# Kernel tuning notes

Hardware: AMD Instinct MI355X
Metric: run time of the kernel (lower is better)

## Reference

```python
import jax, jax.numpy as jnp
import numpy as np

N_NODES = 50000
N_EDGES = 200000
IN_DIM = 512
HID = 2000
LAT = 128


def setup_inputs() -> dict:
    key = jax.random.key(0)
    ks = jax.random.split(key, 6)
    x = jax.random.normal(ks[0], (N_NODES, IN_DIM), dtype=jnp.float32)
    edge_index = jax.random.randint(ks[1], (2, N_EDGES), 0, N_NODES, dtype=jnp.int64)
    # glorot-ish scales so ReLU/Sigmoid stay in a sane range
    W1 = jax.random.normal(ks[2], (IN_DIM, HID), dtype=jnp.float32) * (1.0 / np.sqrt(IN_DIM))
    b1 = jnp.zeros((HID,), dtype=jnp.float32)
    W2 = jax.random.normal(ks[3], (HID, LAT), dtype=jnp.float32) * (1.0 / np.sqrt(HID))
    b2 = jnp.zeros((LAT,), dtype=jnp.float32)
    return {"x": x, "edge_index": edge_index, "W1": W1, "b1": b1, "W2": W2, "b2": b2}


def gcn_conv(x, edge_index, W, b):
    """PyG GCNConv: D^-1/2 (A+I) D^-1/2 (X W) + b, unit edge weights."""
    n = x.shape[0]
    loops = jnp.arange(n, dtype=edge_index.dtype)
    row = jnp.concatenate([edge_index[0], loops])  # source nodes
    col = jnp.concatenate([edge_index[1], loops])  # target nodes
    deg = jax.ops.segment_sum(jnp.ones_like(col, dtype=x.dtype), col, num_segments=n)
    dis = jnp.where(deg > 0, jax.lax.rsqrt(deg), 0.0)  # deg^-1/2, inf -> 0
    norm = dis[row] * dis[col]                         # [E+N]
    h = x @ W                                          # transform first: [N, out]
    msg = h[row] * norm[:, None]                       # gather + normalize: [E+N, out]
    out = jax.ops.segment_sum(msg, col, num_segments=n)  # scatter-add
    return out + b


def reference(x, edge_index, W1, b1, W2, b2):
    h = jax.nn.relu(gcn_conv(x, edge_index, W1, b1))
    return jax.nn.sigmoid(gcn_conv(h, edge_index, W2, b2))
```

## Files before the change

### kernel.cpp

```cpp
#include <hip/hip_runtime.h>
#include <hip/hip_fp16.h>

#define NN 50000
#define NE 200000
#define IND 512
#define HIDD 2000
#define LATD 128

#define M_PAD 50048
#define N1_PAD 2048

typedef _Float16 f16x8 __attribute__((ext_vector_type(8)));
typedef float f32x4 __attribute__((ext_vector_type(4)));

__device__ __forceinline__ void gload_lds16(const _Float16* g, _Float16* l) {
    __builtin_amdgcn_global_load_lds(
        (const __attribute__((address_space(1))) unsigned int*)g,
        (__attribute__((address_space(3))) unsigned int*)l,
        16, 0, 0);
}

__global__ void k_degree(const int* __restrict__ col, int* __restrict__ deg) {
    int e = blockIdx.x * 256 + threadIdx.x;
    if (e < NE) atomicAdd(&deg[col[e]], 1);
}

__global__ void k_dis(const int* __restrict__ deg, float* __restrict__ dis) {
    int i = blockIdx.x * 256 + threadIdx.x;
    if (i < NN) dis[i] = rsqrtf((float)deg[i] + 1.0f);
}

__global__ void k_scan(const int* __restrict__ deg, int* __restrict__ row_ptr) {
    __shared__ int smem[1024];
    const int tid = threadIdx.x;
    int carry = 0;
    for (int chunk = 0; chunk < NN; chunk += 1024) {
        int i = chunk + tid;
        int v = (i < NN) ? deg[i] : 0;
        smem[tid] = v;
        __syncthreads();
        #pragma unroll
        for (int off = 1; off < 1024; off <<= 1) {
            int t = (tid >= off) ? smem[tid - off] : 0;
            __syncthreads();
            if (tid >= off) smem[tid] += t;
            __syncthreads();
        }
        if (i < NN) row_ptr[i] = carry + smem[tid] - v;
        int tot = smem[1023];
        __syncthreads();
        carry += tot;
    }
    if (tid == 0) row_ptr[NN] = carry;
}

__global__ void k_fill(const int* __restrict__ ei, const int* __restrict__ row_ptr,
                       int* __restrict__ cursor, int* __restrict__ csr_src) {
    int e = blockIdx.x * 256 + threadIdx.x;
    if (e < NE) {
        int r = ei[e], c = ei[NE + e];
        int pos = atomicAdd(&cursor[c], 1);
        csr_src[row_ptr[c] + pos] = r;
    }
}

__global__ void k_transpose_cvt(const float* __restrict__ in,
                                _Float16* __restrict__ out, int R, int C, int ldo) {
    int idx = blockIdx.x * 256 + threadIdx.x;
    if (idx < R * C) {
        int r = idx / C, c = idx - r * C;
        out[c * ldo + r] = (_Float16)in[idx];
    }
}

__global__ void k_gather_x(const float* __restrict__ x, const int* __restrict__ row_ptr,
                           const int* __restrict__ csr_src, const float* __restrict__ dis,
                           _Float16* __restrict__ Ah) {
    int dst = blockIdx.x * 4 + (threadIdx.x >> 6);
    if (dst >= NN) return;
    int lane = threadIdx.x & 63;
    float dd = dis[dst];
    const float* xd = x + (size_t)dst * IND + lane * 8;
    float4 a0 = *(const float4*)xd;
    float4 a1 = *(const float4*)(xd + 4);
    float acc[8] = { dd*a0.x, dd*a0.y, dd*a0.z, dd*a0.w,
                     dd*a1.x, dd*a1.y, dd*a1.z, dd*a1.w };
    int beg = row_ptr[dst], end = row_ptr[dst + 1];
    for (int i = beg; i < end; ++i) {
        int s = csr_src[i];
        float ns = dis[s];
        const float* xs = x + (size_t)s * IND + lane * 8;
        float4 b0 = *(const float4*)xs;
        float4 b1 = *(const float4*)(xs + 4);
        acc[0] += ns * b0.x; acc[1] += ns * b0.y; acc[2] += ns * b0.z; acc[3] += ns * b0.w;
        acc[4] += ns * b1.x; acc[5] += ns * b1.y; acc[6] += ns * b1.z; acc[7] += ns * b1.w;
    }
    f16x8 o;
    #pragma unroll
    for (int i = 0; i < 8; ++i) o[i] = (_Float16)(dd * acc[i]);
    *(f16x8*)(Ah + (size_t)dst * IND + lane * 8) = o;
}

__global__ void k_gather_t(const float* __restrict__ t, const int* __restrict__ row_ptr,
                           const int* __restrict__ csr_src, const float* __restrict__ dis,
                           const float* __restrict__ b2, float* __restrict__ out) {
    int dst = blockIdx.x * 4 + (threadIdx.x >> 6);
    if (dst >= NN) return;
    int lane = threadIdx.x & 63;
    float dd = dis[dst];
    float2 td = *(const float2*)(t + (size_t)dst * LATD + lane * 2);
    float accx = dd * td.x, accy = dd * td.y;
    int beg = row_ptr[dst], end = row_ptr[dst + 1];
    for (int i = beg; i < end; ++i) {
        int s = csr_src[i];
        float ns = dis[s];
        float2 ts = *(const float2*)(t + (size_t)s * LATD + lane * 2);
        accx += ns * ts.x; accy += ns * ts.y;
    }
    float2 bb = *(const float2*)(b2 + lane * 2);
    float vx = dd * accx + bb.x;
    float vy = dd * accy + bb.y;
    float2 o;
    o.x = 1.0f / (1.0f + __expf(-vx));
    o.y = 1.0f / (1.0f + __expf(-vy));
    *(float2*)(out + (size_t)dst * LATD + lane * 2) = o;
}

template<bool RELU_BIAS>
__global__ __launch_bounds__(256, 2) void k_gemm_lds(
    const _Float16* __restrict__ A,
    const _Float16* __restrict__ Bt,
    const float* __restrict__ bias,
    _Float16* __restrict__ Ch,
    float* __restrict__ Cf,
    int N, int K)
{
    __shared__ __align__(16) _Float16 As[128 * 32];
    __shared__ __align__(16) _Float16 Bs[128 * 32];

    const int tid = threadIdx.x;
    const int lane = tid & 63;
    const int w = tid >> 6;
    const int mBase = blockIdx.x * 128;
    const int nBase = blockIdx.y * 128;

    const int srow = w * 32 + (lane >> 2);
    const int scol = (lane & 3) * 8;
    const _Float16* Ag0 = A + (size_t)(mBase + srow) * K + scol;
    const _Float16* Ag1 = Ag0 + (size_t)16 * K;
    const _Float16* Bg0 = Bt + (size_t)(nBase + srow) * K + scol;
    const _Float16* Bg1 = Bg0 + (size_t)16 * K;
    _Float16* Asl0 = As + w * 1024;
    _Float16* Asl1 = Asl0 + 512;
    _Float16* Bsl0 = Bs + w * 1024;
    _Float16* Bsl1 = Bsl0 + 512;

    const int wm = (w >> 1) * 64;
    const int wn = (w & 1) * 64;
    const int lm = lane & 15;
    const int quad = lane >> 4;

    f32x4 acc[4][4];
    #pragma unroll
    for (int i = 0; i < 4; ++i)
        #pragma unroll
        for (int j = 0; j < 4; ++j)
            acc[i][j] = (f32x4){0.f, 0.f, 0.f, 0.f};

    for (int k0 = 0; k0 < K; k0 += 32) {
        gload_lds16(Ag0 + k0, Asl0);
        gload_lds16(Ag1 + k0, Asl1);
        gload_lds16(Bg0 + k0, Bsl0);
        gload_lds16(Bg1 + k0, Bsl1);
        __syncthreads();

        f16x8 af[4], bfr[4];
        #pragma unroll
        for (int mi = 0; mi < 4; ++mi)
            af[mi] = *(const f16x8*)&As[(wm + mi * 16 + lm) * 32 + quad * 8];
        #pragma unroll
        for (int ni = 0; ni < 4; ++ni)
            bfr[ni] = *(const f16x8*)&Bs[(wn + ni * 16 + lm) * 32 + quad * 8];
        #pragma unroll
        for (int mi = 0; mi < 4; ++mi)
            #pragma unroll
            for (int ni = 0; ni < 4; ++ni)
                acc[mi][ni] = __builtin_amdgcn_mfma_f32_16x16x32_f16(
                    af[mi], bfr[ni], acc[mi][ni], 0, 0, 0);
        __syncthreads();
    }

    #pragma unroll
    for (int mi = 0; mi < 4; ++mi) {
        #pragma unroll
        for (int ni = 0; ni < 4; ++ni) {
            int col = nBase + wn + ni * 16 + lm;
            float bval = RELU_BIAS ? bias[col] : 0.f;
            #pragma unroll
            for (int r = 0; r < 4; ++r) {
                int rowg = mBase + wm + mi * 16 + quad * 4 + r;
                float v = acc[mi][ni][r];
                if (RELU_BIAS) {
                    v = fmaxf(v + bval, 0.f);
                    Ch[(size_t)rowg * N + col] = (_Float16)v;
                } else {
                    Cf[(size_t)rowg * N + col] = v;
                }
            }
        }
    }
}

extern "C" void kernel_launch(void* const* d_in, const int* in_sizes, int n_in,
                              void* d_out, int out_size, void* d_ws, size_t ws_size,
                              hipStream_t stream) {
    const float* x  = (const float*)d_in[0];
    const int* ei   = (const int*)d_in[1];
    const float* W1 = (const float*)d_in[2];
    const float* b1 = (const float*)d_in[3];
    const float* W2 = (const float*)d_in[4];
    const float* b2 = (const float*)d_in[5];
    float* out = (float*)d_out;

    char* p = (char*)d_ws;
    auto alloc = [&](size_t bytes) {
        char* q = p; p += (bytes + 255) & ~(size_t)255; return q;
    };
    int* deg        = (int*)alloc((size_t)NN * 4);
    int* row_ptr    = (int*)alloc((size_t)(NN + 1) * 4);
    int* cursor     = (int*)alloc((size_t)NN * 4);
    int* csr_src    = (int*)alloc((size_t)NE * 4);
    float* dis      = (float*)alloc((size_t)NN * 4);
    float* b1pad    = (float*)alloc((size_t)N1_PAD * 4);
    _Float16* W1T   = (_Float16*)alloc((size_t)N1_PAD * IND * 2);
    _Float16* W2T   = (_Float16*)alloc((size_t)LATD * N1_PAD * 2);
    _Float16* Ah    = (_Float16*)alloc((size_t)M_PAD * IND * 2);
    _Float16* h     = (_Float16*)alloc((size_t)M_PAD * N1_PAD * 2);
    float* t        = (float*)alloc((size_t)M_PAD * LATD * 4);

    hipMemsetAsync(deg,    0, (size_t)NN * 4, stream);
    hipMemsetAsync(cursor, 0, (size_t)NN * 4, stream);
    hipMemsetAsync(b1pad,  0, (size_t)N1_PAD * 4, stream);
    hipMemsetAsync(W1T,    0, (size_t)N1_PAD * IND * 2, stream);
    hipMemsetAsync(W2T,    0, (size_t)LATD * N1_PAD * 2, stream);
    hipMemcpyAsync(b1pad, b1, (size_t)HIDD * 4, hipMemcpyDeviceToDevice, stream);

    k_degree<<<(NE + 255) / 256, 256, 0, stream>>>(ei + NE, deg);
    k_dis<<<(NN + 255) / 256, 256, 0, stream>>>(deg, dis);
    k_scan<<<1, 1024, 0, stream>>>(deg, row_ptr);
    k_fill<<<(NE + 255) / 256, 256, 0, stream>>>(ei, row_ptr, cursor, csr_src);

    k_transpose_cvt<<<(IND * HIDD + 255) / 256, 256, 0, stream>>>(W1, W1T, IND, HIDD, IND);
    k_transpose_cvt<<<(HIDD * LATD + 255) / 256, 256, 0, stream>>>(W2, W2T, HIDD, LATD, N1_PAD);

    k_gather_x<<<(NN + 3) / 4, 256, 0, stream>>>(x, row_ptr, csr_src, dis, Ah);

    dim3 g1(M_PAD / 128, N1_PAD / 128);
    k_gemm_lds<true><<<g1, 256, 0, stream>>>(Ah, W1T, b1pad, h, nullptr, N1_PAD, IND);
    dim3 g2(M_PAD / 128, LATD / 128);
    k_gemm_lds<false><<<g2, 256, 0, stream>>>(h, W2T, nullptr, nullptr, t, LATD, N1_PAD);

    k_gather_t<<<(NN + 3) / 4, 256, 0, stream>>>(t, row_ptr, csr_src, dis, b2, out);
}
```

Baseline: 620.8 us.

## Fuse both GEMMs into one kernel keeping hidden tile in LDS; convert x to fp16

Replaces the two separate GEMMs with a single fused kernel. Each block computes a 64-row tile of the hidden layer in 128-column chunks, applies bias and ReLU into LDS, and immediately multiplies by a prepacked W2 chunk. This avoids writing and re-reading the large fp16 hidden matrix in global memory. Separately, x is converted to fp16 up front so the neighbour gather reads half the bytes, and the weight transposes now use tiled or prepacked layouts. The fused kernel uses much more LDS per block (about 61 KB), which may limit occupancy. It also recomputes nothing but serialises the two GEMM stages within each block.

Result: no change. 631.3 us (+1.7%).

```diff
diff --git a/kernel.cpp b/kernel.cpp
--- a/kernel.cpp
+++ b/kernel.cpp
@@ -9,8 +9,10 @@
 
 #define M_PAD 50048
 #define N1_PAD 2048
+#define HT_LD 136
 
 typedef _Float16 f16x8 __attribute__((ext_vector_type(8)));
+typedef _Float16 f16x4 __attribute__((ext_vector_type(4)));
 typedef float f32x4 __attribute__((ext_vector_type(4)));
 
 __device__ __forceinline__ void gload_lds16(const _Float16* g, _Float16* l) {
@@ -64,36 +66,65 @@
     }
 }
 
-__global__ void k_transpose_cvt(const float* __restrict__ in,
-                                _Float16* __restrict__ out, int R, int C, int ldo) {
+__global__ void k_transpose_tiled(const float* __restrict__ in,
+                                  _Float16* __restrict__ out, int R, int C, int ldo) {
+    __shared__ float sm[32][33];
+    int c0 = blockIdx.x * 32, r0 = blockIdx.y * 32;
+    int tx = threadIdx.x & 31, ty = threadIdx.x >> 5;
+    #pragma unroll
+    for (int i = 0; i < 4; ++i) {
+        int r = r0 + ty + i * 8, c = c0 + tx;
+        sm[ty + i * 8][tx] = (r < R && c < C) ? in[(size_t)r * C + c] : 0.f;
+    }
+    __syncthreads();
+    #pragma unroll
+    for (int i = 0; i < 4; ++i) {
+        int c = c0 + ty + i * 8, r = r0 + tx;
+        if (c < C && r < R) out[(size_t)c * ldo + r] = (_Float16)sm[tx][ty + i * 8];
+    }
+}
+
+__global__ void k_w2c(const float* __restrict__ W2, _Float16* __restrict__ W2C) {
     int idx = blockIdx.x * 256 + threadIdx.x;
-    if (idx < R * C) {
-        int r = idx / C, c = idx - r * C;
-        out[c * ldo + r] = (_Float16)in[idx];
-    }
-}
-
-__global__ void k_gather_x(const float* __restrict__ x, const int* __restrict__ row_ptr,
+    if (idx >= 16 * 4 * 128 * 32) return;
+    int kk  = idx & 31;
+    int lat = (idx >> 5) & 127;
+    int ki  = (idx >> 12) & 3;
+    int j   = idx >> 14;
+    int hid = j * 128 + ki * 32 + kk;
+    W2C[idx] = (hid < HIDD) ? (_Float16)W2[(size_t)hid * LATD + lat] : (_Float16)0.f;
+}
+
+__global__ void k_xcvt(const float* __restrict__ in, _Float16* __restrict__ out, int n8) {
+    int i = blockIdx.x * 256 + threadIdx.x;
+    if (i < n8) {
+        float4 a = ((const float4*)in)[i * 2];
+        float4 b = ((const float4*)in)[i * 2 + 1];
+        f16x8 o;
+        o[0] = (_Float16)a.x; o[1] = (_Float16)a.y; o[2] = (_Float16)a.z; o[3] = (_Float16)a.w;
+        o[4] = (_Float16)b.x; o[5] = (_Float16)b.y; o[6] = (_Float16)b.z; o[7] = (_Float16)b.w;
+        ((f16x8*)out)[i] = o;
+    }
+}
+
+__global__ void k_gather_x(const _Float16* __restrict__ xh, const int* __restrict__ row_ptr,
                            const int* __restrict__ csr_src, const float* __restrict__ dis,
                            _Float16* __restrict__ Ah) {
     int dst = blockIdx.x * 4 + (threadIdx.x >> 6);
     if (dst >= NN) return;
     int lane = threadIdx.x & 63;
     float dd = dis[dst];
-    const float* xd = x + (size_t)dst * IND + lane * 8;
-    float4 a0 = *(const float4*)xd;
-    float4 a1 = *(const float4*)(xd + 4);
-    float acc[8] = { dd*a0.x, dd*a0.y, dd*a0.z, dd*a0.w,
-                     dd*a1.x, dd*a1.y, dd*a1.z, dd*a1.w };
+    f16x8 sv = *(const f16x8*)(xh + (size_t)dst * IND + lane * 8);
+    float acc[8];
+    #pragma unroll
+    for (int i = 0; i < 8; ++i) acc[i] = dd * (float)sv[i];
     int beg = row_ptr[dst], end = row_ptr[dst + 1];
     for (int i = beg; i < end; ++i) {
         int s = csr_src[i];
         float ns = dis[s];
-        const float* xs = x + (size_t)s * IND + lane * 8;
-        float4 b0 = *(const float4*)xs;
-        float4 b1 = *(const float4*)(xs + 4);
-        acc[0] += ns * b0.x; acc[1] += ns * b0.y; acc[2] += ns * b0.z; acc[3] += ns * b0.w;
-        acc[4] += ns * b1.x; acc[5] += ns * b1.y; acc[6] += ns * b1.z; acc[7] += ns * b1.w;
+        f16x8 v = *(const f16x8*)(xh + (size_t)s * IND + lane * 8);
+        #pragma unroll
+        for (int q = 0; q < 8; ++q) acc[q] += ns * (float)v[q];
     }
     f16x8 o;
     #pragma unroll
@@ -126,87 +157,126 @@
     *(float2*)(out + (size_t)dst * LATD + lane * 2) = o;
 }
 
-template<bool RELU_BIAS>
-__global__ __launch_bounds__(256, 2) void k_gemm_lds(
-    const _Float16* __restrict__ A,
-    const _Float16* __restrict__ Bt,
-    const float* __restrict__ bias,
-    _Float16* __restrict__ Ch,
-    float* __restrict__ Cf,
-    int N, int K)
+__global__ __launch_bounds__(256, 2) void k_fused(
+    const _Float16* __restrict__ Ah,
+    const _Float16* __restrict__ W1C,
+    const float* __restrict__ b1p,
+    const _Float16* __restrict__ W2C,
+    float* __restrict__ t)
 {
-    __shared__ __align__(16) _Float16 As[128 * 32];
-    __shared__ __align__(16) _Float16 Bs[128 * 32];
+    __shared__ __align__(16) _Float16 As[2 * 64 * 32];
+    __shared__ __align__(16) _Float16 Bs[2 * 128 * 32];
+    __shared__ __align__(16) _Float16 W2s[4 * 128 * 32];
+    __shared__ __align__(16) _Float16 ht[64 * HT_LD];
 
     const int tid = threadIdx.x;
     const int lane = tid & 63;
     const int w = tid >> 6;
-    const int mBase = blockIdx.x * 128;
-    const int nBase = blockIdx.y * 128;
-
-    const int srow = w * 32 + (lane >> 2);
-    const int scol = (lane & 3) * 8;
-    const _Float16* Ag0 = A + (size_t)(mBase + srow) * K + scol;
-    const _Float16* Ag1 = Ag0 + (size_t)16 * K;
-    const _Float16* Bg0 = Bt + (size_t)(nBase + srow) * K + scol;
-    const _Float16* Bg1 = Bg0 + (size_t)16 * K;
-    _Float16* Asl0 = As + w * 1024;
-    _Float16* Asl1 = Asl0 + 512;
-    _Float16* Bsl0 = Bs + w * 1024;
-    _Float16* Bsl1 = Bsl0 + 512;
-
-    const int wm = (w >> 1) * 64;
-    const int wn = (w & 1) * 64;
+    const int mBase = blockIdx.x * 64;
     const int lm = lane & 15;
     const int quad = lane >> 4;
 
-    f32x4 acc[4][4];
+    const int wA = (w >> 1) * 64;
+    const int wB = (w & 1) * 32;
+
+    const _Float16* AgBase = Ah + (size_t)(mBase + w * 16 + (lane >> 2)) * IND + (lane & 3) * 8;
+    const _Float16* BgBase = W1C + (size_t)(w * 32 + (lane >> 2)) * IND + (lane & 3) * 8;
+    const _Float16* W2gBase = W2C + w * 4096 + lane * 8;
+    _Float16* AsD  = As + w * 512;
+    _Float16* BsD  = Bs + w * 1024;
+    _Float16* W2sD = W2s + w * 4096;
+
+    f32x4 acc2[4][2];
     #pragma unroll
     for (int i = 0; i < 4; ++i)
         #pragma unroll
-        for (int j = 0; j < 4; ++j)
-            acc[i][j] = (f32x4){0.f, 0.f, 0.f, 0.f};
-
-    for (int k0 = 0; k0 < K; k0 += 32) {
-        gload_lds16(Ag0 + k0, Asl0);
-        gload_lds16(Ag1 + k0, Asl1);
-        gload_lds16(Bg0 + k0, Bsl0);
-        gload_lds16(Bg1 + k0, Bsl1);
+        for (int j = 0; j < 2; ++j)
+            acc2[i][j] = (f32x4){0.f, 0.f, 0.f, 0.f};
+
+    for (int j = 0; j < 16; ++j) {
+        #pragma unroll
+        for (int i = 0; i < 8; ++i)
+            gload_lds16(W2gBase + (size_t)j * 16384 + i * 512, W2sD + i * 512);
+
+        f32x4 acc1[4][2];
+        #pragma unroll
+        for (int mi = 0; mi < 4; ++mi)
+            #pragma unroll
+            for (int ni = 0; ni < 2; ++ni)
+                acc1[mi][ni] = (f32x4){0.f, 0.f, 0.f, 0.f};
+
+        for (int k0 = 0; k0 < IND; k0 += 64) {
+            #pragma unroll
+            for (int s = 0; s < 2; ++s) {
+                gload_lds16(AgBase + k0 + s * 32, AsD + s * 2048);
+                #pragma unroll
+                for (int g = 0; g < 2; ++g)
+                    gload_lds16(BgBase + (size_t)(j * 128 + g * 16) * IND + k0 + s * 32,
+                                BsD + s * 4096 + g * 512);
+            }
+            __syncthreads();
+            #pragma unroll
+            for (int s = 0; s < 2; ++s) {
+                f16x8 wf[4], af[2];
+                #pragma unroll
+                for (int mi = 0; mi < 4; ++mi)
+                    wf[mi] = *(const f16x8*)&Bs[s * 4096 + (wA + mi * 16 + lm) * 32 + quad * 8];
+                #pragma unroll
+                for (int ni = 0; ni < 2; ++ni)
+                    af[ni] = *(const f16x8*)&As[s * 2048 + (wB + ni * 16 + lm) * 32 + quad * 8];
+                #pragma unroll
+                for (int mi = 0; mi < 4; ++mi)
+                    #pragma unroll
+                    for (int ni = 0; ni < 2; ++ni)
+                        acc1[mi][ni] = __builtin_amdgcn_mfma_f32_16x16x32_f16(
+                            wf[mi], af[ni], acc1[mi][ni], 0, 0, 0);
+            }
+            __syncthreads();
+        }
+
+        #pragma unroll
+        for (int mi = 0; mi < 4; ++mi) {
+            int hc0 = wA + mi * 16 + quad * 4;
+            float4 b4 = *(const float4*)&b1p[j * 128 + hc0];
+            #pragma unroll
+            for (int ni = 0; ni < 2; ++ni) {
+                int hrow = wB + ni * 16 + lm;
+                f16x4 pk;
+                pk[0] = (_Float16)fmaxf(acc1[mi][ni][0] + b4.x, 0.f);
+                pk[1] = (_Float16)fmaxf(acc1[mi][ni][1] + b4.y, 0.f);
+                pk[2] = (_Float16)fmaxf(acc1[mi][ni][2] + b4.z, 0.f);
+                pk[3] = (_Float16)fmaxf(acc1[mi][ni][3] + b4.w, 0.f);
+                *(f16x4*)&ht[hrow * HT_LD + hc0] = pk;
+            }
+        }
         __syncthreads();
 
-        f16x8 af[4], bfr[4];
-        #pragma unroll
-        for (int mi = 0; mi < 4; ++mi)
-            af[mi] = *(const f16x8*)&As[(wm + mi * 16 + lm) * 32 + quad * 8];
-        #pragma unroll
-        for (int ni = 0; ni < 4; ++ni)
-            bfr[ni] = *(const f16x8*)&Bs[(wn + ni * 16 + lm) * 32 + quad * 8];
-        #pragma unroll
-        for (int mi = 0; mi < 4; ++mi)
-            #pragma unroll
-            for (int ni = 0; ni < 4; ++ni)
-                acc[mi][ni] = __builtin_amdgcn_mfma_f32_16x16x32_f16(
-                    af[mi], bfr[ni], acc[mi][ni], 0, 0, 0);
+        #pragma unroll
+        for (int ki = 0; ki < 4; ++ki) {
+            f16x8 w2f[4], hf[2];
+            #pragma unroll
+            for (int mi = 0; mi < 4; ++mi)
+                w2f[mi] = *(const f16x8*)&W2s[ki * 4096 + (wA + mi * 16 + lm) * 32 + quad * 8];
+            #pragma unroll
+            for (int ni = 0; ni < 2; ++ni)
+                hf[ni] = *(const f16x8*)&ht[(wB + ni * 16 + lm) * HT_LD + ki * 32 + quad * 8];
+            #pragma unroll
+            for (int mi = 0; mi < 4; ++mi)
+                #pragma unroll
+                for (int ni = 0; ni < 2; ++ni)
+                    acc2[mi][ni] = __builtin_amdgcn_mfma_f32_16x16x32_f16(
+                        w2f[mi], hf[ni], acc2[mi][ni], 0, 0, 0);
+        }
         __syncthreads();
     }
 
     #pragma unroll
     for (int mi = 0; mi < 4; ++mi) {
-        #pragma unroll
-        for (int ni = 0; ni < 4; ++ni) {
-            int col = nBase + wn + ni * 16 + lm;
-            float bval = RELU_BIAS ? bias[col] : 0.f;
-            #pragma unroll
-            for (int r = 0; r < 4; ++r) {
-                int rowg = mBase + wm + mi * 16 + quad * 4 + r;
-                float v = acc[mi][ni][r];
-                if (RELU_BIAS) {
-                    v = fmaxf(v + bval, 0.f);
-                    Ch[(size_t)rowg * N + col] = (_Float16)v;
-                } else {
-                    Cf[(size_t)rowg * N + col] = v;
-                }
-            }
+        int lat0 = wA + mi * 16 + quad * 4;
+        #pragma unroll
+        for (int ni = 0; ni < 2; ++ni) {
+            int m = mBase + wB + ni * 16 + lm;
+            *(f32x4*)&t[(size_t)m * LATD + lat0] = acc2[mi][ni];
         }
     }
 }
@@ -232,17 +302,16 @@
     int* csr_src    = (int*)alloc((size_t)NE * 4);
     float* dis      = (float*)alloc((size_t)NN * 4);
     float* b1pad    = (float*)alloc((size_t)N1_PAD * 4);
-    _Float16* W1T   = (_Float16*)alloc((size_t)N1_PAD * IND * 2);
-    _Float16* W2T   = (_Float16*)alloc((size_t)LATD * N1_PAD * 2);
+    _Float16* W1C   = (_Float16*)alloc((size_t)N1_PAD * IND * 2);
+    _Float16* W2Cb  = (_Float16*)alloc((size_t)16 * 4 * 128 * 32 * 2);
+    _Float16* xh    = (_Float16*)alloc((size_t)NN * IND * 2);
     _Float16* Ah    = (_Float16*)alloc((size_t)M_PAD * IND * 2);
-    _Float16* h     = (_Float16*)alloc((size_t)M_PAD * N1_PAD * 2);
     float* t        = (float*)alloc((size_t)M_PAD * LATD * 4);
 
     hipMemsetAsync(deg,    0, (size_t)NN * 4, stream);
     hipMemsetAsync(cursor, 0, (size_t)NN * 4, stream);
     hipMemsetAsync(b1pad,  0, (size_t)N1_PAD * 4, stream);
-    hipMemsetAsync(W1T,    0, (size_t)N1_PAD * IND * 2, stream);
-    hipMemsetAsync(W2T,    0, (size_t)LATD * N1_PAD * 2, stream);
+    hipMemsetAsync(W1C,    0, (size_t)N1_PAD * IND * 2, stream);
     hipMemcpyAsync(b1pad, b1, (size_t)HIDD * 4, hipMemcpyDeviceToDevice, stream);
 
     k_degree<<<(NE + 255) / 256, 256, 0, stream>>>(ei + NE, deg);
@@ -250,15 +319,16 @@
     k_scan<<<1, 1024, 0, stream>>>(deg, row_ptr);
     k_fill<<<(NE + 255) / 256, 256, 0, stream>>>(ei, row_ptr, cursor, csr_src);
 
-    k_transpose_cvt<<<(IND * HIDD + 255) / 256, 256, 0, stream>>>(W1, W1T, IND, HIDD, IND);
-    k_transpose_cvt<<<(HIDD * LATD + 255) / 256, 256, 0, stream>>>(W2, W2T, HIDD, LATD, N1_PAD);
-
-    k_gather_x<<<(NN + 3) / 4, 256, 0, stream>>>(x, row_ptr, csr_src, dis, Ah);
-
-    dim3 g1(M_PAD / 128, N1_PAD / 128);
-    k_gemm_lds<true><<<g1, 256, 0, stream>>>(Ah, W1T, b1pad, h, nullptr, N1_PAD, IND);
-    dim3 g2(M_PAD / 128, LATD / 128);
-    k_gemm_lds<false><<<g2, 256, 0, stream>>>(h, W2T, nullptr, nullptr, t, LATD, N1_PAD);
+    {
+        dim3 gt1((HIDD + 31) / 32, (IND + 31) / 32);
+        k_transpose_tiled<<<gt1, 256, 0, stream>>>(W1, W1C, IND, HIDD, IND);
+        k_w2c<<<(16 * 4 * 128 * 32 + 255) / 256, 256, 0, stream>>>(W2, W2Cb);
+        k_xcvt<<<(NN * IND / 8 + 255) / 256, 256, 0, stream>>>(x, xh, NN * IND / 8);
+    }
+
+    k_gather_x<<<(NN + 3) / 4, 256, 0, stream>>>(xh, row_ptr, csr_src, dis, Ah);
+
+    k_fused<<<M_PAD / 64, 256, 0, stream>>>(Ah, W1C, b1pad, W2Cb, t);
 
     k_gather_t<<<(NN + 3) / 4, 256, 0, stream>>>(t, row_ptr, csr_src, dis, b2, out);
 }
```
